# Optimization experiments

Measured on AMD Instinct MI355X. Metric: run time of the kernel, lower is better.

## Reference

```python
import jax, jax.numpy as jnp
import numpy as np

M, H, F, T, IT, NUM_SEM = 256, 256, 256, 4, 2, 50
NEG = jnp.float32(-1e30)


def _lin(k, fi, fo):
    kw, kb = jax.random.split(k)
    s = 1.0 / np.sqrt(fi)
    W = jax.random.uniform(kw, (fi, fo), minval=-s, maxval=s, dtype=jnp.float32)
    b = jax.random.uniform(kb, (fo,), minval=-s, maxval=s, dtype=jnp.float32)
    return W, b


def setup_inputs() -> dict:
    key = jax.random.key(0)
    ks = jax.random.split(key, 16)
    parent_feature = jax.random.normal(ks[0], (1, F), dtype=jnp.float32)
    gt_children_code = jax.random.normal(ks[1], (1, 16), dtype=jnp.float32)
    gt_num_code = jax.random.normal(ks[2], (1, 10), dtype=jnp.float32)
    W_parent, b_parent = _lin(ks[3], F + 26, H * M)
    W_exists, b_exists = _lin(ks[4], H, 1)
    W_sem, b_sem = _lin(ks[5], H, NUM_SEM)
    W_el, b_el = _lin(ks[6], 2 * H, H)          # mlp_edge_latent
    s = 1.0 / np.sqrt(H)
    W_ee = jax.random.uniform(ks[7], (T, H), minval=-s, maxval=s, dtype=jnp.float32)  # stacked mlp_edge_exists
    b_ee = jax.random.uniform(ks[8], (T,), minval=-s, maxval=s, dtype=jnp.float32)
    s2 = 1.0 / np.sqrt(3 * H + T)
    W_ne = jax.random.uniform(ks[9], (IT, 3 * H + T, H), minval=-s2, maxval=s2, dtype=jnp.float32)  # node_edge_op
    b_ne = jax.random.uniform(ks[10], (IT, H), minval=-s2, maxval=s2, dtype=jnp.float32)
    W_child, b_child = _lin(ks[11], H * (IT + 1), H)
    W_child2, b_child2 = _lin(ks[12], H, F)
    return dict(parent_feature=parent_feature, gt_children_code=gt_children_code,
                gt_num_code=gt_num_code, W_parent=W_parent, b_parent=b_parent,
                W_exists=W_exists, b_exists=b_exists, W_sem=W_sem, b_sem=b_sem,
                W_el=W_el, b_el=b_el, W_ee=W_ee, b_ee=b_ee, W_ne=W_ne, b_ne=b_ne,
                W_child=W_child, b_child=b_child, W_child2=W_child2, b_child2=b_child2)


def reference(parent_feature, gt_children_code, gt_num_code, W_parent, b_parent,
              W_exists, b_exists, W_sem, b_sem, W_el, b_el, W_ee, b_ee,
              W_ne, b_ne, W_child, b_child, W_child2, b_child2):
    x = jnp.concatenate([parent_feature, gt_children_code, gt_num_code], axis=1)  # [1, F+26]
    child = jax.nn.relu(x @ W_parent + b_parent).reshape(1, M, H)
    exists_logits = child @ W_exists + b_exists                   # [1, M, 1]
    cf = child[0]                                                 # [M, H]
    # edge latents: relu(Linear(cat(cf_i, cf_j))) without materializing [M,M,2H]
    a = cf @ W_el[:H]
    b2 = cf @ W_el[H:]
    el = jax.nn.relu(a[:, None, :] + b2[None, :, :] + b_el)       # [M, M, H]
    ee = jnp.einsum('mnh,th->mnt', el, W_ee) + b_ee               # [M, M, T]
    # fixed edge set: candidate edges where type-logit>0 and both endpoints exist
    node_ok = exists_logits[0, :, 0] > 0                          # [M]
    mask = (ee > 0) & node_ok[:, None, None] & node_ok[None, :, None]  # [M, M, T]
    has_edges = mask.any()
    iter_feats = [cf]
    for i in range(IT):
        W = W_ne[i]
        Ws, Wd, We, Wt = W[:H], W[H:2 * H], W[2 * H:3 * H], W[3 * H:]
        pre = (cf @ Ws)[:, None, :] + (cf @ Wd)[None, :, :] \
              + jnp.einsum('mnh,hk->mnk', el, We) + b_ne[i]       # [M, M, H]
        # one-hot edge-type logit contribution: etl[e,t]=ee[i,j,t] only at the edge's type
        feats = jax.nn.relu(pre[:, :, None, :] + jnp.einsum('mnt,th->mnth', ee, Wt))  # [M,M,T,H]
        # scatter_max over source node i with zero-initialized output
        new = jnp.max(jnp.where(mask[..., None], feats, NEG), axis=(1, 2))  # [M, H]
        new = jnp.maximum(new, 0.0)
        cf = jnp.where(has_edges, new, cf)
        iter_feats.append(cf)
    cfc = jnp.concatenate(iter_feats, axis=1)                     # [M, H*(IT+1)]
    ch = jax.nn.relu(cfc @ W_child + b_child)                     # [M, H]
    child_sem_logits = (ch @ W_sem + b_sem)[None]                 # [1, M, NUM_SEM]
    child_feats = jax.nn.relu(ch @ W_child2 + b_child2)[None]     # [1, M, F]
    return child_feats, child_sem_logits, exists_logits, ee[None]
```

## Files before the change

kernel.cpp:

```cpp
#include <hip/hip_runtime.h>
#include <hip/hip_bf16.h>
#include <stdint.h>

#define NEGV -1e30f

typedef __attribute__((ext_vector_type(8))) __bf16 bf16x8;
typedef __attribute__((ext_vector_type(4))) float f32x4;

__device__ __forceinline__ uint16_t f2bfu(float f){
  __hip_bfloat16 h = __float2bfloat16(f);
  return *reinterpret_cast<const uint16_t*>(&h);
}

__device__ __forceinline__ void dev_transpose(
  const float* __restrict__ in, __hip_bfloat16* __restrict__ out,
  int K, int N, int ktiles, int b, int tid, float* t)
{
  int kt = b % ktiles, nt = b / ktiles;
  int k0 = kt*64, n0 = nt*64;
  int c = tid & 63, rg = tid >> 6;
  #pragma unroll
  for (int rr = 0; rr < 16; ++rr){
    int row = rg + rr*4;
    t[row*65 + c] = in[(k0+row)*N + n0 + c];
  }
  __syncthreads();
  #pragma unroll
  for (int rr = 0; rr < 16; ++rr){
    int row = rg + rr*4;
    out[(n0+row)*K + k0 + c] = __float2bfloat16(t[c*65 + row]);
  }
}

__global__ __launch_bounds__(256) void k_front(
    const float* __restrict__ pf, const float* __restrict__ gc,
    const float* __restrict__ gn, const float* __restrict__ Wp,
    const float* __restrict__ Wne, const float* __restrict__ Wch,
    const float* __restrict__ Wc2, const float* __restrict__ Wsem,
    float* __restrict__ pchild, __hip_bfloat16* __restrict__ WeT,
    __hip_bfloat16* __restrict__ WchT, __hip_bfloat16* __restrict__ Wc2T,
    __hip_bfloat16* __restrict__ WsemT)
{
  __shared__ float sh[64*65];
  int bid = blockIdx.x, tid = threadIdx.x;
  if (bid < 512){
    int jb = bid & 63, ks = bid >> 6;
    int i0 = ks*36, i1 = (i0+36 < 282) ? i0+36 : 282;
    if (tid < i1-i0){
      int i = i0 + tid;
      sh[tid] = (i < 256) ? pf[i] : ((i < 272) ? gc[i-256] : gn[i-272]);
    }
    __syncthreads();
    int j0 = jb*1024 + tid*4;
    f32x4 acc = {0,0,0,0};
    #pragma unroll 6
    for (int i = i0; i < i1; ++i){
      f32x4 w = *reinterpret_cast<const f32x4*>(Wp + i*65536 + j0);
      float x = sh[i-i0];
      acc[0] = fmaf(x, w[0], acc[0]);
      acc[1] = fmaf(x, w[1], acc[1]);
      acc[2] = fmaf(x, w[2], acc[2]);
      acc[3] = fmaf(x, w[3], acc[3]);
    }
    *reinterpret_cast<f32x4*>(pchild + ks*65536 + j0) = acc;
  } else if (bid < 544){
    int b = bid - 512; int it = b >> 4;
    dev_transpose(Wne + it*197632 + 512*256, WeT + it*65536, 256, 256, 4, b & 15, tid, sh);
  } else if (bid < 592){
    dev_transpose(Wch, WchT, 768, 256, 12, bid - 544, tid, sh);
  } else if (bid < 608){
    dev_transpose(Wc2, Wc2T, 256, 256, 4, bid - 592, tid, sh);
  } else {
    int b = bid - 608;
    int j = b*4 + (tid>>6), c = tid & 63;
    float v = (c < 50) ? Wsem[j*50+c] : 0.f;
    WsemT[c*256 + j] = __float2bfloat16(v);
  }
}

__global__ __launch_bounds__(256) void k_child_reduce_exists(
  const float* __restrict__ pchild, const float* __restrict__ bp,
  const float* __restrict__ Wex, const float* __restrict__ bex,
  float* __restrict__ cf, __hip_bfloat16* __restrict__ cfcb,
  float* __restrict__ exout, int* __restrict__ ok, int* __restrict__ flag)
{
  __shared__ float red[256];
  int m = blockIdx.x, tid = threadIdx.x;
  int j = m*256 + tid;
  float s = bp[j];
  #pragma unroll
  for (int ks = 0; ks < 8; ++ks) s += pchild[ks*65536 + j];
  s = fmaxf(s, 0.f);
  cf[j] = s;
  cfcb[m*768 + tid] = __float2bfloat16(s);
  red[tid] = s * Wex[tid];
  __syncthreads();
  for (int st = 128; st > 0; st >>= 1){ if (tid < st) red[tid] += red[tid+st]; __syncthreads(); }
  if (tid == 0){
    float logit = red[0] + bex[0];
    exout[m] = logit;
    ok[m] = logit > 0.f ? 1 : 0;
    if (m == 0) *flag = 0;
  }
}

__global__ __launch_bounds__(256) void k_ab(
  const float* __restrict__ cf, const float* __restrict__ Wel,
  float* __restrict__ a, float* __restrict__ b2)
{
  __shared__ float cfs[2][256];
  int bid = blockIdx.x; int sel = bid >> 7; int m0 = (bid & 127)*2; int tid = threadIdx.x;
  cfs[0][tid] = cf[m0*256 + tid];
  cfs[1][tid] = cf[(m0+1)*256 + tid];
  __syncthreads();
  const float* W = Wel + sel*65536;
  float acc0 = 0.f, acc1 = 0.f;
  #pragma unroll 8
  for (int j = 0; j < 256; ++j){
    float w = W[j*256+tid];
    acc0 = fmaf(cfs[0][j], w, acc0);
    acc1 = fmaf(cfs[1][j], w, acc1);
  }
  float* dst = sel ? b2 : a;
  dst[m0*256+tid] = acc0;
  dst[(m0+1)*256+tid] = acc1;
}

__global__ __launch_bounds__(256) void k_elpack_ee(
  const float* __restrict__ a, const float* __restrict__ b2,
  const float* __restrict__ bel, const float* __restrict__ Wee,
  const float* __restrict__ bee, const int* __restrict__ ok,
  __hip_bfloat16* __restrict__ elp, float* __restrict__ eeout,
  float* __restrict__ eemask, int* __restrict__ flag)
{
  __shared__ float acs[256];
  __shared__ float wee[1024];
  int bid = blockIdx.x; int m = bid >> 2, nt = bid & 3;
  int tid = threadIdx.x;
  acs[tid] = a[m*256+tid] + bel[tid];
  #pragma unroll
  for (int p = 0; p < 4; ++p) wee[p*256+tid] = Wee[p*256+tid];
  __syncthreads();
  int w = tid>>6, l = tid&63, l15 = l&15, lg = l>>4;
  int T = m*16 + nt*4 + w;
  int n = nt*64 + w*16 + l15;
  const float* br = b2 + (size_t)n*256;
  char* outb = reinterpret_cast<char*>(elp) + (size_t)T*8192 + (size_t)l*16;
  float e[4] = {0.f,0.f,0.f,0.f};
  #pragma unroll
  for (int kk = 0; kk < 8; ++kk){
    int h0 = kk*32 + lg*8;
    f32x4 bb0 = *reinterpret_cast<const f32x4*>(br + h0);
    f32x4 bb1 = *reinterpret_cast<const f32x4*>(br + h0 + 4);
    f32x4 aa0 = *reinterpret_cast<const f32x4*>(acs + h0);
    f32x4 aa1 = *reinterpret_cast<const f32x4*>(acs + h0 + 4);
    float el[8];
    #pragma unroll
    for (int j = 0; j < 4; ++j){
      el[j]   = fmaxf(aa0[j]+bb0[j], 0.f);
      el[j+4] = fmaxf(aa1[j]+bb1[j], 0.f);
    }
    union { uint16_t u[8]; bf16x8 v; } fr;
    #pragma unroll
    for (int j = 0; j < 8; ++j) fr.u[j] = f2bfu(el[j]);
    *reinterpret_cast<bf16x8*>(outb + kk*1024) = fr.v;
    #pragma unroll
    for (int t = 0; t < 4; ++t){
      f32x4 w0 = *reinterpret_cast<const f32x4*>(&wee[t*256+h0]);
      f32x4 w1 = *reinterpret_cast<const f32x4*>(&wee[t*256+h0+4]);
      e[t] += el[0]*w0[0] + el[1]*w0[1] + el[2]*w0[2] + el[3]*w0[3]
            + el[4]*w1[0] + el[5]*w1[1] + el[6]*w1[2] + el[7]*w1[3];
    }
  }
  #pragma unroll
  for (int t = 0; t < 4; ++t){
    float v = e[t];
    v += __shfl_xor(v, 16);
    v += __shfl_xor(v, 32);
    e[t] = v + bee[t];
  }
  bool valid = false;
  if (lg == 0){
    int okmn = ok[m] & ok[n];
    f32x4 eo, em;
    #pragma unroll
    for (int t = 0; t < 4; ++t){
      eo[t] = e[t];
      em[t] = (okmn && e[t] > 0.f) ? e[t] : NEGV;
      valid = valid || (em[t] > -1e29f);
    }
    int idx = (m*256+n)*4;
    *reinterpret_cast<f32x4*>(eeout + idx) = eo;
    *reinterpret_cast<f32x4*>(eemask + idx) = em;
  }
  if (__any(valid) && l == 0) atomicOr(flag, 1);
}

__global__ __launch_bounds__(256) void k_sd(
  const float* __restrict__ cf, const float* __restrict__ Wne,
  const float* __restrict__ bne, float* __restrict__ sp, float* __restrict__ d, int it)
{
  __shared__ float cfs[2][256];
  int bid = blockIdx.x; int sel = bid >> 7; int m0 = (bid & 127)*2; int tid = threadIdx.x;
  cfs[0][tid] = cf[m0*256 + tid];
  cfs[1][tid] = cf[(m0+1)*256 + tid];
  __syncthreads();
  const float* W = Wne + it*197632 + sel*65536;
  float bias = sel ? 0.f : bne[it*256+tid];
  float acc0 = bias, acc1 = bias;
  #pragma unroll 8
  for (int j = 0; j < 256; ++j){
    float w = W[j*256+tid];
    acc0 = fmaf(cfs[0][j], w, acc0);
    acc1 = fmaf(cfs[1][j], w, acc1);
  }
  float* dst = sel ? d : sp;
  dst[m0*256+tid] = acc0;
  dst[(m0+1)*256+tid] = acc1;
}

__global__ __launch_bounds__(256,2) void k_fused_elp(
  const __hip_bfloat16* __restrict__ elp, const __hip_bfloat16* __restrict__ wet,
  const float* __restrict__ sp, const float* __restrict__ dmat,
  const float* __restrict__ eemask, const float* __restrict__ Wne_it,
  float* __restrict__ cf, __hip_bfloat16* __restrict__ cfcb,
  const int* __restrict__ flag, int it)
{
  __shared__ __attribute__((aligned(16))) char weS[32768];
  __shared__ float red[4][64];
  int bid = blockIdx.x; int m = bid >> 2, kc = bid & 3;
  int tid = threadIdx.x;
  const char* wsrc = reinterpret_cast<const char*>(wet + kc*16384);
  #pragma unroll
  for (int p = 0; p < 8; ++p){
    int i = p*256 + tid;
    int row = i >> 5, colb = (i & 31) << 4;
    int byte = (row << 9) | colb;
    *reinterpret_cast<bf16x8*>(weS + (byte ^ ((row & 7) << 4))) =
      *reinterpret_cast<const bf16x8*>(wsrc + byte);
  }
  __syncthreads();

  int w = tid >> 6, l = tid & 63, l15 = l & 15, lg = l >> 4;
  float spv[4], wtv[4][4];
  #pragma unroll
  for (int kt = 0; kt < 4; ++kt){
    int kcol = kc*64 + kt*16 + l15;
    spv[kt] = sp[m*256+kcol];
    #pragma unroll
    for (int t = 0; t < 4; ++t) wtv[t][kt] = Wne_it[(768+t)*256 + kcol];
  }
  int rowb[4], rowx[4];
  #pragma unroll
  for (int kt = 0; kt < 4; ++kt){
    int row = kt*16 + l15;
    rowb[kt] = row << 9;
    rowx[kt] = (row & 7) << 4;
  }
  float runmax[4] = {NEGV, NEGV, NEGV, NEGV};

  for (int ni = 0; ni < 4; ++ni){
    int nb = w*64 + ni*16;
    int T = m*16 + w*4 + ni;
    const char* ap = reinterpret_cast<const char*>(elp) + (size_t)T*8192 + (size_t)l*16;
    f32x4 me[4];
    float dv[4][4];
    #pragma unroll
    for (int r = 0; r < 4; ++r){
      int n = nb + lg*4 + r;
      me[r] = *reinterpret_cast<const f32x4*>(eemask + (m*256+n)*4);
      const float* dr = dmat + n*256 + kc*64;
      #pragma unroll
      for (int kt = 0; kt < 4; ++kt) dv[r][kt] = dr[kt*16 + l15];
    }
    bf16x8 Af[8];
    #pragma unroll
    for (int kk = 0; kk < 8; ++kk)
      Af[kk] = *reinterpret_cast<const bf16x8*>(ap + kk*1024);

    f32x4 acc0 = {0,0,0,0}, acc1 = {0,0,0,0}, acc2 = {0,0,0,0}, acc3 = {0,0,0,0};
    #pragma unroll
    for (int kk = 0; kk < 8; ++kk){
      int c = kk*64 + lg*16;
      bf16x8 B0 = *reinterpret_cast<const bf16x8*>(weS + ((rowb[0] + c) ^ rowx[0]));
      bf16x8 B1 = *reinterpret_cast<const bf16x8*>(weS + ((rowb[1] + c) ^ rowx[1]));
      bf16x8 B2 = *reinterpret_cast<const bf16x8*>(weS + ((rowb[2] + c) ^ rowx[2]));
      bf16x8 B3 = *reinterpret_cast<const bf16x8*>(weS + ((rowb[3] + c) ^ rowx[3]));
      acc0 = __builtin_amdgcn_mfma_f32_16x16x32_bf16(Af[kk], B0, acc0, 0, 0, 0);
      acc1 = __builtin_amdgcn_mfma_f32_16x16x32_bf16(Af[kk], B1, acc1, 0, 0, 0);
      acc2 = __builtin_amdgcn_mfma_f32_16x16x32_bf16(Af[kk], B2, acc2, 0, 0, 0);
      acc3 = __builtin_amdgcn_mfma_f32_16x16x32_bf16(Af[kk], B3, acc3, 0, 0, 0);
    }
    #pragma unroll
    for (int r = 0; r < 4; ++r){
      float Ed0 = acc0[r] + dv[r][0] + spv[0];
      float Ed1 = acc1[r] + dv[r][1] + spv[1];
      float Ed2 = acc2[r] + dv[r][2] + spv[2];
      float Ed3 = acc3[r] + dv[r][3] + spv[3];
      #pragma unroll
      for (int t = 0; t < 4; ++t){
        if (me[r][t] > -1e29f){
          runmax[0] = fmaxf(runmax[0], fmaf(me[r][t], wtv[t][0], Ed0));
          runmax[1] = fmaxf(runmax[1], fmaf(me[r][t], wtv[t][1], Ed1));
          runmax[2] = fmaxf(runmax[2], fmaf(me[r][t], wtv[t][2], Ed2));
          runmax[3] = fmaxf(runmax[3], fmaf(me[r][t], wtv[t][3], Ed3));
        }
      }
    }
  }
  #pragma unroll
  for (int kt = 0; kt < 4; ++kt){
    float v = runmax[kt];
    v = fmaxf(v, __shfl_xor(v, 16));
    v = fmaxf(v, __shfl_xor(v, 32));
    if (l < 16) red[w][kt*16 + l] = v;
  }
  __syncthreads();
  if (tid < 64){
    float v = fmaxf(fmaxf(red[0][tid], red[1][tid]), fmaxf(red[2][tid], red[3][tid]));
    float nv = fmaxf(v, 0.f);
    int kcol = kc*64 + tid;
    float outv = (*flag) ? nv : cf[m*256+kcol];
    cf[m*256+kcol] = outv;
    cfcb[m*768 + 256*(it+1) + kcol] = __float2bfloat16(outv);
  }
}

__global__ __launch_bounds__(256) void k_final_mfma(
  const __hip_bfloat16* __restrict__ cfcb, const __hip_bfloat16* __restrict__ WchT,
  const float* __restrict__ bch, const __hip_bfloat16* __restrict__ Wc2T,
  const float* __restrict__ bc2, const __hip_bfloat16* __restrict__ WsemT,
  const float* __restrict__ bsem, float* __restrict__ feats_out,
  float* __restrict__ sem_out)
{
  __shared__ char chs[8192];
  int tid = threadIdx.x; int w = tid>>6, l = tid&63, l15 = l&15, lg = l>>4;
  int m0 = blockIdx.x*16;

  f32x4 acc[4] = {{0,0,0,0},{0,0,0,0},{0,0,0,0},{0,0,0,0}};
  const __hip_bfloat16* Aptr = cfcb + (m0 + l15)*768;
  #pragma unroll 2
  for (int ks = 0; ks < 24; ++ks){
    int k0 = ks*32 + lg*8;
    bf16x8 Af = *reinterpret_cast<const bf16x8*>(Aptr + k0);
    #pragma unroll
    for (int nt = 0; nt < 4; ++nt){
      int col = w*64 + nt*16 + l15;
      bf16x8 Bf = *reinterpret_cast<const bf16x8*>(WchT + col*768 + k0);
      acc[nt] = __builtin_amdgcn_mfma_f32_16x16x32_bf16(Af, Bf, acc[nt], 0, 0, 0);
    }
  }
  #pragma unroll
  for (int nt = 0; nt < 4; ++nt){
    int col = w*64 + nt*16 + l15;
    float bias = bch[col];
    #pragma unroll
    for (int r = 0; r < 4; ++r){
      int row = lg*4 + r;
      float v = fmaxf(acc[nt][r] + bias, 0.f);
      int byte = ((row*256 + col)*2) ^ ((row&7)<<4);
      *reinterpret_cast<__hip_bfloat16*>(chs + byte) = __float2bfloat16(v);
    }
  }
  __syncthreads();

  f32x4 accf[4] = {{0,0,0,0},{0,0,0,0},{0,0,0,0},{0,0,0,0}};
  f32x4 accs = {0,0,0,0};
  int cols_sem = w*16 + l15;
  #pragma unroll 2
  for (int ks = 0; ks < 8; ++ks){
    int k0 = ks*32 + lg*8;
    int byteA = (l15*512 + k0*2) ^ ((l15&7)<<4);
    bf16x8 Af = *reinterpret_cast<const bf16x8*>(chs + byteA);
    #pragma unroll
    for (int nt = 0; nt < 4; ++nt){
      int col = w*64 + nt*16 + l15;
      bf16x8 Bf = *reinterpret_cast<const bf16x8*>(Wc2T + col*256 + k0);
      accf[nt] = __builtin_amdgcn_mfma_f32_16x16x32_bf16(Af, Bf, accf[nt], 0, 0, 0);
    }
    bf16x8 Bs = *reinterpret_cast<const bf16x8*>(WsemT + cols_sem*256 + k0);
    accs = __builtin_amdgcn_mfma_f32_16x16x32_bf16(Af, Bs, accs, 0, 0, 0);
  }
  #pragma unroll
  for (int nt = 0; nt < 4; ++nt){
    int col = w*64 + nt*16 + l15;
    float bias = bc2[col];
    #pragma unroll
    for (int r = 0; r < 4; ++r){
      int row = m0 + lg*4 + r;
      feats_out[row*256 + col] = fmaxf(accf[nt][r] + bias, 0.f);
    }
  }
  if (cols_sem < 50){
    float bias = bsem[cols_sem];
    #pragma unroll
    for (int r = 0; r < 4; ++r){
      int row = m0 + lg*4 + r;
      sem_out[row*50 + cols_sem] = accs[r] + bias;
    }
  }
}

extern "C" void kernel_launch(void* const* d_in, const int* in_sizes, int n_in,
                              void* d_out, int out_size, void* d_ws, size_t ws_size,
                              hipStream_t stream)
{
  const float* pf  = (const float*)d_in[0];
  const float* gc  = (const float*)d_in[1];
  const float* gn  = (const float*)d_in[2];
  const float* Wp  = (const float*)d_in[3];
  const float* bp  = (const float*)d_in[4];
  const float* Wex = (const float*)d_in[5];
  const float* bex = (const float*)d_in[6];
  const float* Wsem= (const float*)d_in[7];
  const float* bsem= (const float*)d_in[8];
  const float* Wel = (const float*)d_in[9];
  const float* bel = (const float*)d_in[10];
  const float* Wee = (const float*)d_in[11];
  const float* bee = (const float*)d_in[12];
  const float* Wne = (const float*)d_in[13];
  const float* bne = (const float*)d_in[14];
  const float* Wch = (const float*)d_in[15];
  const float* bch = (const float*)d_in[16];
  const float* Wc2 = (const float*)d_in[17];
  const float* bc2 = (const float*)d_in[18];

  float* out = (float*)d_out;
  float* feats_out = out;
  float* sem_out   = out + 65536;
  float* ex_out    = out + 78336;
  float* ee_out    = out + 78592;

  char* ws = (char*)d_ws;
  float* cf    = (float*)(ws);
  float* a_    = (float*)(ws + ( 256u<<10));
  float* b2_   = (float*)(ws + ( 512u<<10));
  float* sp_   = (float*)(ws + (1024u<<10));
  float* dmat  = (float*)(ws + (1280u<<10));
  float* eem   = (float*)(ws + (1536u<<10));
  __hip_bfloat16* WeT   = (__hip_bfloat16*)(ws + (2560u<<10));
  __hip_bfloat16* cfcb  = (__hip_bfloat16*)(ws + (2816u<<10));
  __hip_bfloat16* WchT  = (__hip_bfloat16*)(ws + (3200u<<10));
  __hip_bfloat16* Wc2T  = (__hip_bfloat16*)(ws + (3584u<<10));
  __hip_bfloat16* WsemT = (__hip_bfloat16*)(ws + (3712u<<10));
  int* ok   = (int*)(ws + (3744u<<10));
  int* flag = ok + 256;
  float* pchild = (float*)(ws + (3776u<<10));
  __hip_bfloat16* elp = (__hip_bfloat16*)(ws + (6144u<<10));

  k_front<<<672,256,0,stream>>>(pf,gc,gn,Wp,Wne,Wch,Wc2,Wsem,
                                pchild,WeT,WchT,Wc2T,WsemT);
  k_child_reduce_exists<<<256,256,0,stream>>>(pchild,bp,Wex,bex,cf,cfcb,ex_out,ok,flag);
  k_ab<<<256,256,0,stream>>>(cf,Wel,a_,b2_);
  k_elpack_ee<<<1024,256,0,stream>>>(a_,b2_,bel,Wee,bee,ok,elp,ee_out,eem,flag);
  for (int it = 0; it < 2; ++it){
    k_sd<<<256,256,0,stream>>>(cf,Wne,bne,sp_,dmat,it);
    k_fused_elp<<<1024,256,0,stream>>>(elp,WeT + it*65536,sp_,dmat,eem,
                                       Wne + it*197632,cf,cfcb,flag,it);
  }
  k_final_mfma<<<16,256,0,stream>>>(cfcb,WchT,bch,Wc2T,bc2,WsemT,bsem,feats_out,sem_out);
}
```

Measured before the change: 174.0 us.

## Recompute edge latents in LDS inside fused kernel instead of materializing bf16 buffer

The edge kernel no longer writes the packed bf16 edge-latent tensor (M*M*H) to global memory. Instead, each fused iteration block rebuilds its 64-row edge-latent chunk in shared memory from the per-node a/b projections, using relu(a+b) with a swizzled layout, and feeds the MFMA from there. This removes a 32 MB write and two 32 MB reads per run. In exchange, every block redoes the elementwise work once per iteration and per column chunk (4x redundancy across kc), needs an extra 32 KB of LDS that may lower occupancy, and adds block barriers.

```diff
diff --git a/kernel.cpp b/kernel.cpp
--- a/kernel.cpp
+++ b/kernel.cpp
@@ -126,12 +126,11 @@
   dst[(m0+1)*256+tid] = acc1;
 }
 
-__global__ __launch_bounds__(256) void k_elpack_ee(
+__global__ __launch_bounds__(256) void k_ee(
   const float* __restrict__ a, const float* __restrict__ b2,
   const float* __restrict__ bel, const float* __restrict__ Wee,
   const float* __restrict__ bee, const int* __restrict__ ok,
-  __hip_bfloat16* __restrict__ elp, float* __restrict__ eeout,
-  float* __restrict__ eemask, int* __restrict__ flag)
+  float* __restrict__ eeout, float* __restrict__ eemask, int* __restrict__ flag)
 {
   __shared__ float acs[256];
   __shared__ float wee[1024];
@@ -142,10 +141,8 @@
   for (int p = 0; p < 4; ++p) wee[p*256+tid] = Wee[p*256+tid];
   __syncthreads();
   int w = tid>>6, l = tid&63, l15 = l&15, lg = l>>4;
-  int T = m*16 + nt*4 + w;
   int n = nt*64 + w*16 + l15;
   const float* br = b2 + (size_t)n*256;
-  char* outb = reinterpret_cast<char*>(elp) + (size_t)T*8192 + (size_t)l*16;
   float e[4] = {0.f,0.f,0.f,0.f};
   #pragma unroll
   for (int kk = 0; kk < 8; ++kk){
@@ -160,10 +157,6 @@
       el[j]   = fmaxf(aa0[j]+bb0[j], 0.f);
       el[j+4] = fmaxf(aa1[j]+bb1[j], 0.f);
     }
-    union { uint16_t u[8]; bf16x8 v; } fr;
-    #pragma unroll
-    for (int j = 0; j < 8; ++j) fr.u[j] = f2bfu(el[j]);
-    *reinterpret_cast<bf16x8*>(outb + kk*1024) = fr.v;
     #pragma unroll
     for (int t = 0; t < 4; ++t){
       f32x4 w0 = *reinterpret_cast<const f32x4*>(&wee[t*256+h0]);
@@ -219,17 +212,21 @@
   dst[(m0+1)*256+tid] = acc1;
 }
 
-__global__ __launch_bounds__(256,2) void k_fused_elp(
-  const __hip_bfloat16* __restrict__ elp, const __hip_bfloat16* __restrict__ wet,
+__global__ __launch_bounds__(256,2) void k_fused_v3(
+  const float* __restrict__ a, const float* __restrict__ bel,
+  const float* __restrict__ b2, const __hip_bfloat16* __restrict__ wet,
   const float* __restrict__ sp, const float* __restrict__ dmat,
   const float* __restrict__ eemask, const float* __restrict__ Wne_it,
   float* __restrict__ cf, __hip_bfloat16* __restrict__ cfcb,
   const int* __restrict__ flag, int it)
 {
   __shared__ __attribute__((aligned(16))) char weS[32768];
+  __shared__ __attribute__((aligned(16))) char elS[32768];
+  __shared__ float acs[256];
   __shared__ float red[4][64];
   int bid = blockIdx.x; int m = bid >> 2, kc = bid & 3;
   int tid = threadIdx.x;
+  acs[tid] = a[m*256+tid] + bel[tid];
   const char* wsrc = reinterpret_cast<const char*>(wet + kc*16384);
   #pragma unroll
   for (int p = 0; p < 8; ++p){
@@ -257,12 +254,27 @@
     rowb[kt] = row << 9;
     rowx[kt] = (row & 7) << 4;
   }
+  int arow = w*16 + l15;
+  int abase = (arow << 9) ^ ((arow & 7) << 4);
   float runmax[4] = {NEGV, NEGV, NEGV, NEGV};
 
-  for (int ni = 0; ni < 4; ++ni){
-    int nb = w*64 + ni*16;
-    int T = m*16 + w*4 + ni;
-    const char* ap = reinterpret_cast<const char*>(elp) + (size_t)T*8192 + (size_t)l*16;
+  for (int c = 0; c < 4; ++c){
+    #pragma unroll
+    for (int p = 0; p < 16; ++p){
+      int idx = p*256 + tid;
+      int row = idx >> 6;
+      int h4 = (idx & 63) << 2;
+      f32x4 bv = *reinterpret_cast<const f32x4*>(b2 + (size_t)(c*64+row)*256 + h4);
+      f32x4 av = *reinterpret_cast<const f32x4*>(acs + h4);
+      union { uint16_t u[4]; uint64_t d; } pk;
+      #pragma unroll
+      for (int j = 0; j < 4; ++j) pk.u[j] = f2bfu(fmaxf(av[j]+bv[j], 0.f));
+      int byte = (row << 9) | (h4 << 1);
+      *reinterpret_cast<uint64_t*>(elS + (byte ^ ((row & 7) << 4))) = pk.d;
+    }
+    __syncthreads();
+
+    int nb = c*64 + w*16;
     f32x4 me[4];
     float dv[4][4];
     #pragma unroll
@@ -276,16 +288,16 @@
     bf16x8 Af[8];
     #pragma unroll
     for (int kk = 0; kk < 8; ++kk)
-      Af[kk] = *reinterpret_cast<const bf16x8*>(ap + kk*1024);
+      Af[kk] = *reinterpret_cast<const bf16x8*>(elS + (((arow << 9) | (kk*64 + lg*16)) ^ ((arow & 7) << 4)));
 
     f32x4 acc0 = {0,0,0,0}, acc1 = {0,0,0,0}, acc2 = {0,0,0,0}, acc3 = {0,0,0,0};
     #pragma unroll
     for (int kk = 0; kk < 8; ++kk){
-      int c = kk*64 + lg*16;
-      bf16x8 B0 = *reinterpret_cast<const bf16x8*>(weS + ((rowb[0] + c) ^ rowx[0]));
-      bf16x8 B1 = *reinterpret_cast<const bf16x8*>(weS + ((rowb[1] + c) ^ rowx[1]));
-      bf16x8 B2 = *reinterpret_cast<const bf16x8*>(weS + ((rowb[2] + c) ^ rowx[2]));
-      bf16x8 B3 = *reinterpret_cast<const bf16x8*>(weS + ((rowb[3] + c) ^ rowx[3]));
+      int cc = kk*64 + lg*16;
+      bf16x8 B0 = *reinterpret_cast<const bf16x8*>(weS + ((rowb[0] + cc) ^ rowx[0]));
+      bf16x8 B1 = *reinterpret_cast<const bf16x8*>(weS + ((rowb[1] + cc) ^ rowx[1]));
+      bf16x8 B2 = *reinterpret_cast<const bf16x8*>(weS + ((rowb[2] + cc) ^ rowx[2]));
+      bf16x8 B3 = *reinterpret_cast<const bf16x8*>(weS + ((rowb[3] + cc) ^ rowx[3]));
       acc0 = __builtin_amdgcn_mfma_f32_16x16x32_bf16(Af[kk], B0, acc0, 0, 0, 0);
       acc1 = __builtin_amdgcn_mfma_f32_16x16x32_bf16(Af[kk], B1, acc1, 0, 0, 0);
       acc2 = __builtin_amdgcn_mfma_f32_16x16x32_bf16(Af[kk], B2, acc2, 0, 0, 0);
@@ -307,6 +319,7 @@
         }
       }
     }
+    __syncthreads();
   }
   #pragma unroll
   for (int kt = 0; kt < 4; ++kt){
@@ -446,17 +459,16 @@
   int* ok   = (int*)(ws + (3744u<<10));
   int* flag = ok + 256;
   float* pchild = (float*)(ws + (3776u<<10));
-  __hip_bfloat16* elp = (__hip_bfloat16*)(ws + (6144u<<10));
 
   k_front<<<672,256,0,stream>>>(pf,gc,gn,Wp,Wne,Wch,Wc2,Wsem,
                                 pchild,WeT,WchT,Wc2T,WsemT);
   k_child_reduce_exists<<<256,256,0,stream>>>(pchild,bp,Wex,bex,cf,cfcb,ex_out,ok,flag);
   k_ab<<<256,256,0,stream>>>(cf,Wel,a_,b2_);
-  k_elpack_ee<<<1024,256,0,stream>>>(a_,b2_,bel,Wee,bee,ok,elp,ee_out,eem,flag);
+  k_ee<<<1024,256,0,stream>>>(a_,b2_,bel,Wee,bee,ok,ee_out,eem,flag);
   for (int it = 0; it < 2; ++it){
     k_sd<<<256,256,0,stream>>>(cf,Wne,bne,sp_,dmat,it);
-    k_fused_elp<<<1024,256,0,stream>>>(elp,WeT + it*65536,sp_,dmat,eem,
-                                       Wne + it*197632,cf,cfcb,flag,it);
+    k_fused_v3<<<1024,256,0,stream>>>(a_,bel,b2_,WeT + it*65536,sp_,dmat,eem,
+                                      Wne + it*197632,cf,cfcb,flag,it);
   }
   k_final_mfma<<<16,256,0,stream>>>(cfcb,WchT,bch,Wc2T,bc2,WsemT,bsem,feats_out,sem_out);
 }
```

Result: no change. 176.1 us (+1.2%).
